# Performance work log

Measured on AMD Instinct MI355X. Metric: run time of the kernel, lower is better.

## Reference

```python
import jax, jax.numpy as jnp
import numpy as np

N, E, G = 50000, 800000, 64
NODE_DIM, HID, HEADS, EDGE_DIM = 128, 256, 4, 2
LAYER_IN = [NODE_DIM, HID, HID]
LAYER_HEADS = [HEADS, HEADS, 1]
BN_EPS = 1e-5


def setup_inputs() -> dict:
    key = jax.random.key(0)
    ks = iter(jax.random.split(key, 80))
    def nrm(shape, s=0.05):
        return jax.random.normal(next(ks), shape, jnp.float32) * s
    inp = {}
    inp['x'] = jax.random.normal(next(ks), (N, NODE_DIM), jnp.float32)
    inp['edge_index'] = jax.random.randint(next(ks), (2, E), 0, N, jnp.int32)
    inp['edge_attr'] = jax.random.normal(next(ks), (E, EDGE_DIM), jnp.float32)
    inp['batch'] = jnp.sort(jax.random.randint(next(ks), (N,), 0, G, jnp.int32))
    for i in range(3):
        H = LAYER_HEADS[i]; C = HID // H
        inp[f'W{i}'] = nrm((LAYER_IN[i], H * C))
        inp[f'asrc{i}'] = nrm((H, C))
        inp[f'adst{i}'] = nrm((H, C))
        inp[f'We{i}'] = nrm((EDGE_DIM, H * C))
        inp[f'aedge{i}'] = nrm((H, C))
        inp[f'bconv{i}'] = jnp.zeros((HID,), jnp.float32)
        inp[f'bn{i}_g'] = jnp.ones((HID,), jnp.float32)
        inp[f'bn{i}_b'] = jnp.zeros((HID,), jnp.float32)
        inp[f'bn{i}_m'] = nrm((HID,), 0.01)
        inp[f'bn{i}_v'] = jnp.ones((HID,), jnp.float32)
    inp['Wskip'] = nrm((NODE_DIM, HID))
    inp['bskip'] = jnp.zeros((HID,), jnp.float32)
    inp['Wp1'] = nrm((2 * HID, HID))
    inp['bp1'] = jnp.zeros((HID,), jnp.float32)
    inp['Wp2'] = nrm((HID, 1))
    inp['bp2'] = jnp.zeros((1,), jnp.float32)
    return inp


def gat_conv(x, src, dst, ea, W, a_s, a_d, We, a_e, b, H, concat):
    n = x.shape[0]
    C = W.shape[1] // H
    h = (x @ W).reshape(n, H, C)                      # [N,H,C]
    # attention logits per edge (src/dst node terms + edge term)
    al = ((h * a_s).sum(-1)[src]
          + (h * a_d).sum(-1)[dst]
          + ((ea @ We).reshape(-1, H, C) * a_e).sum(-1))  # [Et,H]
    al = jax.nn.leaky_relu(al, 0.2)
    # segment softmax over destination nodes
    amax = jax.ops.segment_max(al, dst, num_segments=n)
    ex = jnp.exp(al - amax[dst])
    den = jax.ops.segment_sum(ex, dst, num_segments=n)
    alpha = ex / (den[dst] + 1e-16)
    out = jax.ops.segment_sum(h[src] * alpha[..., None], dst, num_segments=n)  # [N,H,C]
    out = out.reshape(n, H * C) if concat else out.mean(axis=1)
    return out + b


def _forward(x, edge_index, edge_attr, batch, layer_params, Wskip, bskip, Wp1, bp1, Wp2, bp2):
    n = x.shape[0]
    # add self-loops (PyG GATConv default), edge_attr filled with mean
    loop = jnp.arange(n, dtype=edge_index.dtype)
    src = jnp.concatenate([edge_index[0], loop])
    dst = jnp.concatenate([edge_index[1], loop])
    ea = jnp.concatenate([edge_attr, jnp.broadcast_to(edge_attr.mean(0), (n, edge_attr.shape[1]))], axis=0)
    identity = x
    for i, (W, a_s, a_d, We, a_e, b, g, be, rm, rv) in enumerate(layer_params):
        layer_identity = (identity @ Wskip + bskip) if i == 0 else identity
        concat = i < 2
        H = LAYER_HEADS[i]
        h = gat_conv(x, src, dst, ea, W, a_s, a_d, We, a_e, b, H, concat)
        h = (h - rm) * jax.lax.rsqrt(rv + BN_EPS) * g + be   # BatchNorm1d (eval)
        h = jax.nn.elu(h)
        x = h + layer_identity
        identity = x
    # global mean + max pool per graph
    counts = jnp.maximum(jax.ops.segment_sum(jnp.ones((n,), x.dtype), batch, num_segments=G), 1.0)
    mean_pool = jax.ops.segment_sum(x, batch, num_segments=G) / counts[:, None]
    max_pool = jax.ops.segment_max(x, batch, num_segments=G)
    emb = jnp.concatenate([mean_pool, max_pool], axis=1)      # [G, 2*HID]
    hmid = jax.nn.relu(emb @ Wp1 + bp1)
    return hmid @ Wp2 + bp2                                   # [G, 1]


def reference(x, edge_index, edge_attr, batch,
              W0, asrc0, adst0, We0, aedge0, bconv0, bn0_g, bn0_b, bn0_m, bn0_v,
              W1, asrc1, adst1, We1, aedge1, bconv1, bn1_g, bn1_b, bn1_m, bn1_v,
              W2, asrc2, adst2, We2, aedge2, bconv2, bn2_g, bn2_b, bn2_m, bn2_v,
              Wskip, bskip, Wp1, bp1, Wp2, bp2):
    layer_params = [
        (W0, asrc0, adst0, We0, aedge0, bconv0, bn0_g, bn0_b, bn0_m, bn0_v),
        (W1, asrc1, adst1, We1, aedge1, bconv1, bn1_g, bn1_b, bn1_m, bn1_v),
        (W2, asrc2, adst2, We2, aedge2, bconv2, bn2_g, bn2_b, bn2_m, bn2_v),
    ]
    return _forward(x, edge_index, edge_attr, batch, layer_params, Wskip, bskip, Wp1, bp1, Wp2, bp2)
```

## Files before the change

kernel.cpp:

```cpp
#include <hip/hip_runtime.h>
#include <cfloat>

#define Nn 50000
#define Ee 800000
#define Etot (Ee + Nn)
#define Gg 64
#define HIDc 256
#define BN_EPS 1e-5f

typedef unsigned int   uint32;
typedef unsigned short ushort16;
typedef short  bf16x8 __attribute__((ext_vector_type(8)));
typedef float  f32x4  __attribute__((ext_vector_type(4)));

__device__ inline ushort16 f2bf(float f) {
    uint32 u = __float_as_uint(f);
    u = (u + 0x7fffu + ((u >> 16) & 1u)) >> 16;
    return (ushort16)u;
}
__device__ inline uint32 pack2(float a, float b) {
    return (uint32)f2bf(a) | ((uint32)f2bf(b) << 16);
}
__device__ inline uint32 fenc(float f) {
    uint32 b = __float_as_uint(f);
    return (b & 0x80000000u) ? ~b : (b | 0x80000000u);
}
__device__ inline float fdec(uint32 u) {
    uint32 b = (u & 0x80000000u) ? (u & 0x7fffffffu) : ~u;
    return __uint_as_float(b);
}

__device__ inline long ws_index(int c, int k, int KB) {
    int cb = c >> 4, m = c & 15, kb = k >> 5, q = (k >> 3) & 3, e = k & 7;
    return (((long)(cb * KB + kb) * 64 + q * 16 + m) << 3) + e;
}

#define CVT4 (Nn * 128 / 4)
#define CVT_BLKS ((CVT4 + 255) / 256)
#define EBKS ((Etot + 255) / 256)
__global__ __launch_bounds__(256) void prep_kernel(
        const float* __restrict__ ea, float* __restrict__ ea_s,
        const float* __restrict__ We0, const float* __restrict__ ae0,
        const float* __restrict__ We1, const float* __restrict__ ae1,
        const float* __restrict__ We2, const float* __restrict__ ae2,
        float* __restrict__ M,
        const float* __restrict__ W0, const float* __restrict__ Wskip,
        const float* __restrict__ W1, const float* __restrict__ W2,
        ushort16* __restrict__ WtC, ushort16* __restrict__ Wt1,
        ushort16* __restrict__ Wt2,
        const float* __restrict__ x, ushort16* __restrict__ xbf,
        const int* __restrict__ ei, int* __restrict__ counts) {
    int bid = blockIdx.x, t = threadIdx.x;
    if (bid < 256) {
        __shared__ float sh0[256], sh1[256];
        float s0 = 0.f, s1 = 0.f;
        for (int e = bid * 256 + t; e < Ee; e += 256 * 256) {
            s0 += ea[2 * e];
            s1 += ea[2 * e + 1];
        }
        sh0[t] = s0; sh1[t] = s1;
        __syncthreads();
        for (int off = 128; off > 0; off >>= 1) {
            if (t < off) { sh0[t] += sh0[t + off]; sh1[t] += sh1[t + off]; }
            __syncthreads();
        }
        if (t == 0) { atomicAdd(&ea_s[0], sh0[0]); atomicAdd(&ea_s[1], sh1[0]); }
    } else if (bid == 256) {
        if (t >= 18) return;
        int l = t < 8 ? 0 : (t < 16 ? 1 : 2);
        int r = t - l * 8;
        const float* We = (l == 0) ? We0 : (l == 1 ? We1 : We2);
        const float* ae = (l == 0) ? ae0 : (l == 1 ? ae1 : ae2);
        int Hl = (l < 2) ? 4 : 1;
        int Cl = 256 / Hl;
        int d = r / Hl, hh = r % Hl;
        float s = 0.f;
        for (int c = 0; c < Cl; ++c)
            s += We[d * 256 + hh * Cl + c] * ae[hh * Cl + c];
        M[l * 8 + r] = s;
    } else if (bid < 385) {
        int k = bid - 257;
        WtC[ws_index(t, k, 4)] = f2bf(W0[(long)k * 256 + t]);
    } else if (bid < 513) {
        int k = bid - 385;
        WtC[ws_index(256 + t, k, 4)] = f2bf(Wskip[(long)k * 256 + t]);
    } else if (bid < 769) {
        int k = bid - 513;
        Wt1[ws_index(t, k, 8)] = f2bf(W1[(long)k * 256 + t]);
    } else if (bid < 1025) {
        int k = bid - 769;
        Wt2[ws_index(t, k, 8)] = f2bf(W2[(long)k * 256 + t]);
    } else if (bid < 1025 + CVT_BLKS) {
        int i = (bid - 1025) * 256 + t;
        if (i < CVT4) {
            float4 v = *(const float4*)&x[i * 4];
            ushort4 o;
            o.x = f2bf(v.x); o.y = f2bf(v.y); o.z = f2bf(v.z); o.w = f2bf(v.w);
            *(ushort4*)&xbf[i * 4] = o;
        }
    } else {
        int e = (bid - 1025 - CVT_BLKS) * 256 + t;
        if (e < Etot) {
            int d = (e < Ee) ? ei[Ee + e] : (e - Ee);
            atomicAdd(&counts[d], 1);
        }
    }
}

__global__ void scan1_kernel(const int* __restrict__ in, int* __restrict__ inc,
                             int* __restrict__ bsums) {
    __shared__ int sh[256];
    int i = blockIdx.x * 256 + threadIdx.x;
    int v = (i < Nn) ? in[i] : 0;
    sh[threadIdx.x] = v;
    __syncthreads();
    for (int off = 1; off < 256; off <<= 1) {
        int t = ((int)threadIdx.x >= off) ? sh[threadIdx.x - off] : 0;
        __syncthreads();
        sh[threadIdx.x] += t;
        __syncthreads();
    }
    if (i < Nn) inc[i] = sh[threadIdx.x];
    if (threadIdx.x == 255) bsums[blockIdx.x] = sh[255];
}

__global__ void scan23_kernel(const int* __restrict__ inc, const int* __restrict__ bsums,
                              int* __restrict__ row_start, int* __restrict__ cursor, int nb) {
    __shared__ int sh[256];
    int b = blockIdx.x, t = threadIdx.x;
    sh[t] = (t < b && t < nb) ? bsums[t] : 0;
    __syncthreads();
    for (int off = 128; off > 0; off >>= 1) {
        if (t < off) sh[t] += sh[t + off];
        __syncthreads();
    }
    int base = sh[0];
    int i = b * 256 + t;
    if (i < Nn) {
        int v = inc[i] + base;
        row_start[i + 1] = v;
        cursor[i + 1] = v;
    }
    if (i == 0) { row_start[0] = 0; cursor[0] = 0; }
}

__global__ void scatter_kernel(const int* __restrict__ ei, const float* __restrict__ ea,
                               const float* __restrict__ ea_sum, int* __restrict__ cursor,
                               int* __restrict__ src_sorted, float* __restrict__ ea_sorted) {
    int e = blockIdx.x * blockDim.x + threadIdx.x;
    if (e >= Etot) return;
    int s, d; float e0, e1;
    if (e < Ee) {
        s = ei[e]; d = ei[Ee + e];
        e0 = ea[2 * e]; e1 = ea[2 * e + 1];
    } else {
        s = d = e - Ee;
        const float invE = 1.f / (float)Ee;
        e0 = ea_sum[0] * invE; e1 = ea_sum[1] * invE;
    }
    int pos = atomicAdd(&cursor[d], 1);
    src_sorted[pos] = s;
    ea_sorted[2 * pos]     = e0;
    ea_sorted[2 * pos + 1] = e1;
}

#define LDK 40
__global__ __launch_bounds__(256) void mfma_gemm_kernel(
        const ushort16* __restrict__ A,
        const ushort16* __restrict__ WS,
        uint32* __restrict__ outF,
        uint32* __restrict__ outS,
        const float* __restrict__ bskip,
        const float* __restrict__ a_s, const float* __restrict__ a_d,
        float* __restrict__ ssrc, float* __restrict__ sdst,
        int n, int K) {
    __shared__ ushort16 As[128 * LDK];
    const int t    = threadIdx.x;
    const int row0 = blockIdx.x * 128;
    const int c0   = blockIdx.y * 128;
    const bool isSkip = (outS != nullptr) && (c0 >= 256);
    const int cc0  = isSkip ? c0 - 256 : c0;
    const int wave = t >> 6, lane = t & 63;
    const int wr = wave >> 1, wc = wave & 1;
    const int l15 = lane & 15, quad = lane >> 4;
    const int KB = K >> 5;

    f32x4 acc[4][4];
#pragma unroll
    for (int j = 0; j < 4; ++j)
#pragma unroll
        for (int i = 0; i < 4; ++i) {
            acc[j][i][0] = 0.f; acc[j][i][1] = 0.f;
            acc[j][i][2] = 0.f; acc[j][i][3] = 0.f;
        }

    const int sm = t & 127;
    const int so = t >> 7;

    for (int k0 = 0; k0 < K; k0 += 32) {
        const int kb = k0 >> 5;
#pragma unroll
        for (int h = 0; h < 2; ++h) {
            int oct = so + 2 * h;
            int grow = row0 + sm;
            uint4 va = make_uint4(0, 0, 0, 0);
            if (grow < n) va = *(const uint4*)&A[(long)grow * K + k0 + 8 * oct];
            *(uint4*)&As[sm * LDK + 8 * oct] = va;
        }
        bf16x8 bfv[4];
#pragma unroll
        for (int j = 0; j < 4; ++j) {
            int cb = ((c0 + wc * 64) >> 4) + j;
            bfv[j] = *(const bf16x8*)&WS[(((long)cb * KB + kb) * 64 + lane) << 3];
        }
        __syncthreads();
        bf16x8 af[4];
#pragma unroll
        for (int i = 0; i < 4; ++i)
            af[i] = *(const bf16x8*)&As[(wr * 64 + i * 16 + l15) * LDK + quad * 8];
#pragma unroll
        for (int j = 0; j < 4; ++j)
#pragma unroll
            for (int i = 0; i < 4; ++i)
                acc[j][i] = __builtin_amdgcn_mfma_f32_16x16x32_bf16(
                    bfv[j], af[i], acc[j][i], 0, 0, 0);
        __syncthreads();
    }

    float4 bb[4];
#pragma unroll
    for (int j = 0; j < 4; ++j) {
        if (isSkip) bb[j] = *(const float4*)&bskip[cc0 + wc * 64 + j * 16 + quad * 4];
        else        bb[j] = make_float4(0.f, 0.f, 0.f, 0.f);
    }

    uint32* tgt = isSkip ? outS : outF;
#pragma unroll
    for (int i = 0; i < 4; ++i) {
        int row = row0 + wr * 64 + i * 16 + l15;
        if (row >= n) continue;
#pragma unroll
        for (int j = 0; j < 4; ++j) {
            int col = cc0 + wc * 64 + j * 16 + quad * 4;
            uint2 pk;
            pk.x = pack2(acc[j][i][0] + bb[j].x, acc[j][i][1] + bb[j].y);
            pk.y = pack2(acc[j][i][2] + bb[j].z, acc[j][i][3] + bb[j].w);
            *(uint2*)&tgt[(long)row * 128 + (col >> 1)] = pk;
        }
    }

    if (!isSkip && a_s != nullptr) {
        float4 asv[4], adv[4];
#pragma unroll
        for (int j = 0; j < 4; ++j) {
            int col = cc0 + wc * 64 + j * 16 + quad * 4;
            asv[j] = *(const float4*)&a_s[col];
            adv[j] = *(const float4*)&a_d[col];
        }
        const int part = (cc0 + wc * 64) >> 6;
#pragma unroll
        for (int i = 0; i < 4; ++i) {
            float ps = 0.f, pd = 0.f;
#pragma unroll
            for (int j = 0; j < 4; ++j) {
                ps += acc[j][i][0] * asv[j].x + acc[j][i][1] * asv[j].y
                    + acc[j][i][2] * asv[j].z + acc[j][i][3] * asv[j].w;
                pd += acc[j][i][0] * adv[j].x + acc[j][i][1] * adv[j].y
                    + acc[j][i][2] * adv[j].z + acc[j][i][3] * adv[j].w;
            }
            ps += __shfl_xor(ps, 16); ps += __shfl_xor(ps, 32);
            pd += __shfl_xor(pd, 16); pd += __shfl_xor(pd, 32);
            if (quad == 0) {
                int row = row0 + wr * 64 + i * 16 + l15;
                if (row < n) {
                    ssrc[row * 4 + part] = ps;
                    sdst[row * 4 + part] = pd;
                }
            }
        }
    }
}

template <int H>
__global__ __launch_bounds__(256) void edge_softmax_kernel(
        const int* __restrict__ src_sorted, const int* __restrict__ row_start,
        const float* __restrict__ ea_sorted, const float* __restrict__ ssrc,
        const float* __restrict__ sdst, const float* __restrict__ M,
        float* __restrict__ w) {
    int node = (blockIdx.x * blockDim.x + threadIdx.x) >> 4;
    int l16 = threadIdx.x & 15;
    if (node >= Nn) return;
    int beg = row_start[node], end = row_start[node + 1];
    int deg = end - beg;
    float sd[H], M0[H], M1[H], m[H], den[H];
    if (H == 4) {
#pragma unroll
        for (int h = 0; h < H; ++h) sd[h] = sdst[node * 4 + h];
    } else {
        float4 v = *(const float4*)&sdst[node * 4];
        sd[0] = v.x + v.y + v.z + v.w;
    }
#pragma unroll
    for (int h = 0; h < H; ++h) {
        M0[h] = M[h]; M1[h] = M[H + h];
        m[h] = -FLT_MAX; den[h] = 0.f;
    }
    auto ssval = [&](int s, int h) -> float {
        if (H == 4) return ssrc[s * 4 + h];
        float4 v = *(const float4*)&ssrc[s * 4];
        return v.x + v.y + v.z + v.w;
    };
    if (deg <= 64) {
        float lreg[4][H];
#pragma unroll
        for (int k = 0; k < 4; ++k) {
            int idx = beg + l16 + (k << 4);
            if (idx < end) {
                int s = src_sorted[idx];
                float e0 = ea_sorted[2 * idx], e1 = ea_sorted[2 * idx + 1];
#pragma unroll
                for (int h = 0; h < H; ++h) {
                    float l = ssval(s, h) + sd[h] + e0 * M0[h] + e1 * M1[h];
                    l = (l > 0.f) ? l : 0.2f * l;
                    lreg[k][h] = l;
                    if (l > m[h]) { den[h] = den[h] * __expf(m[h] - l) + 1.f; m[h] = l; }
                    else den[h] += __expf(l - m[h]);
                }
            }
        }
#pragma unroll
        for (int h = 0; h < H; ++h) {
#pragma unroll
            for (int off = 1; off < 16; off <<= 1) {
                float om = __shfl_xor(m[h], off);
                float od = __shfl_xor(den[h], off);
                float nm = fmaxf(m[h], om);
                den[h] = den[h] * __expf(m[h] - nm) + od * __expf(om - nm);
                m[h] = nm;
            }
            den[h] = 1.f / (den[h] + 1e-16f);
        }
#pragma unroll
        for (int k = 0; k < 4; ++k) {
            int idx = beg + l16 + (k << 4);
            if (idx < end) {
#pragma unroll
                for (int h = 0; h < H; ++h)
                    w[(long)idx * H + h] = __expf(lreg[k][h] - m[h]) * den[h];
            }
        }
    } else {
        for (int idx = beg + l16; idx < end; idx += 16) {
            int s = src_sorted[idx];
            float e0 = ea_sorted[2 * idx], e1 = ea_sorted[2 * idx + 1];
#pragma unroll
            for (int h = 0; h < H; ++h) {
                float l = ssval(s, h) + sd[h] + e0 * M0[h] + e1 * M1[h];
                l = (l > 0.f) ? l : 0.2f * l;
                w[(long)idx * H + h] = l;
                if (l > m[h]) { den[h] = den[h] * __expf(m[h] - l) + 1.f; m[h] = l; }
                else den[h] += __expf(l - m[h]);
            }
        }
#pragma unroll
        for (int h = 0; h < H; ++h) {
#pragma unroll
            for (int off = 1; off < 16; off <<= 1) {
                float om = __shfl_xor(m[h], off);
                float od = __shfl_xor(den[h], off);
                float nm = fmaxf(m[h], om);
                den[h] = den[h] * __expf(m[h] - nm) + od * __expf(om - nm);
                m[h] = nm;
            }
            den[h] = 1.f / (den[h] + 1e-16f);
        }
        for (int idx = beg + l16; idx < end; idx += 16) {
#pragma unroll
            for (int h = 0; h < H; ++h) {
                float l = w[(long)idx * H + h];
                w[(long)idx * H + h] = __expf(l - m[h]) * den[h];
            }
        }
    }
}

__global__ __launch_bounds__(128) void agg_kernel(
        const int* __restrict__ src_sorted, const int* __restrict__ row_start,
        const uint32* __restrict__ hbuf2, const float* __restrict__ w,
        const float* __restrict__ bconv,
        const float* __restrict__ bn_g, const float* __restrict__ bn_b,
        const float* __restrict__ bn_m, const float* __restrict__ bn_v,
        const uint32* __restrict__ identity2, uint32* __restrict__ out2, int H) {
    int node = blockIdx.x;
    int c2 = threadIdx.x;
    int C2 = 128 / H;
    int hh = c2 / C2;
    int beg = row_start[node], end = row_start[node + 1];
    float a0 = 0.f, a1 = 0.f;
    for (int idx = beg; idx < end; idx += 4) {
        int   s[4];
        float ww[4];
#pragma unroll
        for (int k = 0; k < 4; ++k) {
            int j = idx + k;
            bool ok = j < end;
            int jj = ok ? j : beg;
            s[k]  = src_sorted[jj];
            ww[k] = ok ? w[(long)jj * H + hh] : 0.f;
        }
#pragma unroll
        for (int k = 0; k < 4; ++k) {
            uint32 u = hbuf2[(long)s[k] * 128 + c2];
            float lo = __uint_as_float(u << 16);
            float hi = __uint_as_float(u & 0xffff0000u);
            a0 += ww[k] * lo;
            a1 += ww[k] * hi;
        }
    }
    int c = 2 * c2;
    float v0 = a0 + bconv[c];
    float v1 = a1 + bconv[c + 1];
    v0 = (v0 - bn_m[c])     * rsqrtf(bn_v[c]     + BN_EPS) * bn_g[c]     + bn_b[c];
    v1 = (v1 - bn_m[c + 1]) * rsqrtf(bn_v[c + 1] + BN_EPS) * bn_g[c + 1] + bn_b[c + 1];
    v0 = (v0 > 0.f) ? v0 : (expf(v0) - 1.f);
    v1 = (v1 > 0.f) ? v1 : (expf(v1) - 1.f);
    uint32 idu = identity2[(long)node * 128 + c2];
    v0 += __uint_as_float(idu << 16);
    v1 += __uint_as_float(idu & 0xffff0000u);
    out2[(long)node * 128 + c2] = pack2(v0, v1);
}

#define POOL_ROWS 32
__global__ __launch_bounds__(128) void pool_kernel(
        const uint32* __restrict__ x2, const int* __restrict__ batch,
        float* __restrict__ psum, uint32* __restrict__ pmax, float* __restrict__ pcnt) {
    int c2 = threadIdx.x;
    int n0 = blockIdx.x * POOL_ROWS;
    if (n0 >= Nn) return;
    int n1 = min(n0 + POOL_ROWS, Nn);
    int cur = batch[n0];
    float s0 = 0.f, s1 = 0.f, m0 = -FLT_MAX, m1 = -FLT_MAX;
    int cnt = 0;
    int c = 2 * c2;
    for (int i = n0; i < n1; ++i) {
        int g = batch[i];
        if (g != cur) {
            atomicAdd(&psum[cur * 256 + c], s0);
            atomicAdd(&psum[cur * 256 + c + 1], s1);
            atomicMax(&pmax[cur * 256 + c], fenc(m0));
            atomicMax(&pmax[cur * 256 + c + 1], fenc(m1));
            if (c2 == 0) atomicAdd(&pcnt[cur], (float)cnt);
            cur = g; s0 = s1 = 0.f; m0 = m1 = -FLT_MAX; cnt = 0;
        }
        uint32 u = x2[(long)i * 128 + c2];
        float lo = __uint_as_float(u << 16);
        float hi = __uint_as_float(u & 0xffff0000u);
        s0 += lo; s1 += hi;
        m0 = fmaxf(m0, lo); m1 = fmaxf(m1, hi);
        ++cnt;
    }
    atomicAdd(&psum[cur * 256 + c], s0);
    atomicAdd(&psum[cur * 256 + c + 1], s1);
    atomicMax(&pmax[cur * 256 + c], fenc(m0));
    atomicMax(&pmax[cur * 256 + c + 1], fenc(m1));
    if (c2 == 0) atomicAdd(&pcnt[cur], (float)cnt);
}

__global__ __launch_bounds__(256) void mlp_kernel(
        const float* __restrict__ psum, const uint32* __restrict__ pmax,
        const float* __restrict__ pcnt, const float* __restrict__ Wp1,
        const float* __restrict__ bp1, const float* __restrict__ Wp2,
        const float* __restrict__ bp2, float* __restrict__ out) {
    int g = blockIdx.x;
    int j = threadIdx.x;
    float inv = 1.f / fmaxf(pcnt[g], 1.f);
    float acc = bp1[j];
    for (int k = 0; k < 256; ++k)
        acc += (psum[g * 256 + k] * inv) * Wp1[k * 256 + j];
    for (int k = 0; k < 256; ++k)
        acc += fdec(pmax[g * 256 + k]) * Wp1[(256 + k) * 256 + j];
    float v = fmaxf(acc, 0.f) * Wp2[j];
    __shared__ float red[256];
    red[j] = v;
    __syncthreads();
    for (int off = 128; off > 0; off >>= 1) {
        if (j < off) red[j] += red[j + off];
        __syncthreads();
    }
    if (j == 0) out[g] = red[0] + bp2[0];
}

extern "C" void kernel_launch(void* const* d_in, const int* in_sizes, int n_in,
                              void* d_out, int out_size, void* d_ws, size_t ws_size,
                              hipStream_t stream) {
    const float* x   = (const float*)d_in[0];
    const int*   ei  = (const int*)d_in[1];
    const float* ea  = (const float*)d_in[2];
    const int*   bat = (const int*)d_in[3];
    auto LP = [&](int l, int j) { return (const float*)d_in[4 + l * 10 + j]; };
    const float* Wskip = (const float*)d_in[34];
    const float* bskip = (const float*)d_in[35];
    const float* Wp1   = (const float*)d_in[36];
    const float* bp1   = (const float*)d_in[37];
    const float* Wp2   = (const float*)d_in[38];
    const float* bp2   = (const float*)d_in[39];
    float* out = (float*)d_out;

    char* p = (char*)d_ws;
    auto alloc = [&](size_t bytes) { void* r = (void*)p; p += (bytes + 255) & ~(size_t)255; return r; };
    uint32*   hbuf2  = (uint32*)alloc((size_t)Nn * 256 * 2);
    uint32*   skipbf = (uint32*)alloc((size_t)Nn * 128 * 4);
    uint32*   resA   = (uint32*)alloc((size_t)Nn * 128 * 4);
    uint32*   resB   = (uint32*)alloc((size_t)Nn * 128 * 4);
    ushort16* xbf    = (ushort16*)alloc((size_t)Nn * 128 * 2);
    float*    wbuf   = (float*)alloc((size_t)Etot * 4 * 4);
    float*    ea_sorted = (float*)alloc((size_t)Etot * 2 * 4);
    float*    ssrc   = (float*)alloc((size_t)Nn * 4 * 4);
    float*    sdst   = (float*)alloc((size_t)Nn * 4 * 4);
    int*      counts = (int*)alloc((size_t)Nn * 4);
    int*      incb   = (int*)alloc((size_t)Nn * 4);
    int*      row_start = (int*)alloc((size_t)(Nn + 1) * 4);
    int*      cursor    = (int*)alloc((size_t)(Nn + 1) * 4);
    int*      src_sorted = (int*)alloc((size_t)Etot * 4);
    int*      bsums  = (int*)alloc(256 * 4);
    float*    ea_s   = (float*)alloc(2 * 4);
    float*    Mbuf   = (float*)alloc(32 * 4);
    ushort16* WtC    = (ushort16*)alloc((size_t)512 * 128 * 2);
    ushort16* Wt1    = (ushort16*)alloc((size_t)256 * 256 * 2);
    ushort16* Wt2    = (ushort16*)alloc((size_t)256 * 256 * 2);
    float*    psum   = (float*)alloc((size_t)Gg * 256 * 4);
    uint32*   pmax   = (uint32*)alloc((size_t)Gg * 256 * 4);
    float*    pcnt   = (float*)alloc((size_t)Gg * 4);

    const int nb = (Nn + 255) / 256;
    const int sgrid = (Nn * 16 + 255) / 256;

    hipMemsetAsync(counts, 0, (size_t)Nn * 4, stream);
    hipMemsetAsync(ea_s, 0, 8, stream);
    hipMemsetAsync(psum, 0, (size_t)Gg * 256 * 4 * 2 + (size_t)Gg * 4, stream);

    prep_kernel<<<1025 + CVT_BLKS + EBKS, 256, 0, stream>>>(
        ea, ea_s, LP(0,3), LP(0,4), LP(1,3), LP(1,4), LP(2,3), LP(2,4), Mbuf,
        LP(0,0), Wskip, LP(1,0), LP(2,0), WtC, Wt1, Wt2, x, xbf, ei, counts);

    scan1_kernel<<<nb, 256, 0, stream>>>(counts, incb, bsums);
    scan23_kernel<<<nb, 256, 0, stream>>>(incb, bsums, row_start, cursor, nb);
    scatter_kernel<<<EBKS, 256, 0, stream>>>(ei, ea, ea_s, cursor, src_sorted, ea_sorted);

    {
        dim3 g0((Nn + 127) / 128, 4);
        mfma_gemm_kernel<<<g0, 256, 0, stream>>>(
            xbf, WtC, hbuf2, skipbf, bskip,
            LP(0,1), LP(0,2), ssrc, sdst, Nn, 128);
    }

    const uint32* lid[3] = { skipbf, resA, resB };
    uint32*       lou[3] = { resA, resB, resA };
    const int     Hh[3]  = { 4, 4, 1 };
    const ushort16* lain[3] = { nullptr, (ushort16*)resA, (ushort16*)resB };
    const ushort16* lwt[3]  = { nullptr, Wt1, Wt2 };
    for (int l = 0; l < 3; ++l) {
        const int H = Hh[l];
        if (l > 0) {
            dim3 gl((Nn + 127) / 128, 2);
            mfma_gemm_kernel<<<gl, 256, 0, stream>>>(
                lain[l], lwt[l], hbuf2, nullptr, nullptr,
                LP(l,1), LP(l,2), ssrc, sdst, Nn, 256);
        }
        if (H == 4)
            edge_softmax_kernel<4><<<sgrid, 256, 0, stream>>>(
                src_sorted, row_start, ea_sorted, ssrc, sdst, Mbuf + l * 8, wbuf);
        else
            edge_softmax_kernel<1><<<sgrid, 256, 0, stream>>>(
                src_sorted, row_start, ea_sorted, ssrc, sdst, Mbuf + l * 8, wbuf);
        agg_kernel<<<Nn, 128, 0, stream>>>(src_sorted, row_start, hbuf2, wbuf,
            LP(l,5), LP(l,6), LP(l,7), LP(l,8), LP(l,9), lid[l], lou[l], H);
    }

    pool_kernel<<<(Nn + POOL_ROWS - 1) / POOL_ROWS, 128, 0, stream>>>(resA, bat, psum, pmax, pcnt);
    mlp_kernel<<<Gg, 256, 0, stream>>>(psum, pmax, pcnt, Wp1, bp1, Wp2, bp2, out);
}
```

Before: 669.0 us.

## Aggregate one node per wavefront with 8-byte loads and deeper unroll

The aggregation kernel now maps one 64-lane wavefront per destination node, with four nodes per 256-thread block, instead of one 128-thread block per node. Each lane loads two packed bf16 pairs (uint2) and accumulates four channels, and the edge loop is unrolled by 8 to keep more gathers in flight. The aim is less per-block launch and scheduling overhead, wider memory transactions and more memory-level parallelism in the gather-bound loop. Register pressure rises, and wavefronts in the same block finish unevenly when node degrees differ.

```diff
diff --git a/kernel.cpp b/kernel.cpp
--- a/kernel.cpp
+++ b/kernel.cpp
@@ -384,50 +384,68 @@
     }
 }
 
-__global__ __launch_bounds__(128) void agg_kernel(
+#define AGG_UNROLL 8
+__global__ __launch_bounds__(256) void agg_kernel(
         const int* __restrict__ src_sorted, const int* __restrict__ row_start,
         const uint32* __restrict__ hbuf2, const float* __restrict__ w,
         const float* __restrict__ bconv,
         const float* __restrict__ bn_g, const float* __restrict__ bn_b,
         const float* __restrict__ bn_m, const float* __restrict__ bn_v,
         const uint32* __restrict__ identity2, uint32* __restrict__ out2, int H) {
-    int node = blockIdx.x;
-    int c2 = threadIdx.x;
-    int C2 = 128 / H;
-    int hh = c2 / C2;
+    int wv = threadIdx.x >> 6;
+    int l  = threadIdx.x & 63;
+    int node = blockIdx.x * 4 + wv;
+    if (node >= Nn) return;
+    int lanesPerHead = 64 / H;
+    int hh = l / lanesPerHead;
     int beg = row_start[node], end = row_start[node + 1];
-    float a0 = 0.f, a1 = 0.f;
-    for (int idx = beg; idx < end; idx += 4) {
-        int   s[4];
-        float ww[4];
-#pragma unroll
-        for (int k = 0; k < 4; ++k) {
+    float a0 = 0.f, a1 = 0.f, a2 = 0.f, a3 = 0.f;
+    for (int idx = beg; idx < end; idx += AGG_UNROLL) {
+        int   s[AGG_UNROLL];
+        float ww[AGG_UNROLL];
+#pragma unroll
+        for (int k = 0; k < AGG_UNROLL; ++k) {
             int j = idx + k;
             bool ok = j < end;
-            int jj = ok ? j : beg;
+            int jj = ok ? j : (end - 1);
             s[k]  = src_sorted[jj];
             ww[k] = ok ? w[(long)jj * H + hh] : 0.f;
         }
 #pragma unroll
-        for (int k = 0; k < 4; ++k) {
-            uint32 u = hbuf2[(long)s[k] * 128 + c2];
-            float lo = __uint_as_float(u << 16);
-            float hi = __uint_as_float(u & 0xffff0000u);
-            a0 += ww[k] * lo;
-            a1 += ww[k] * hi;
-        }
-    }
-    int c = 2 * c2;
-    float v0 = a0 + bconv[c];
-    float v1 = a1 + bconv[c + 1];
-    v0 = (v0 - bn_m[c])     * rsqrtf(bn_v[c]     + BN_EPS) * bn_g[c]     + bn_b[c];
-    v1 = (v1 - bn_m[c + 1]) * rsqrtf(bn_v[c + 1] + BN_EPS) * bn_g[c + 1] + bn_b[c + 1];
+        for (int k = 0; k < AGG_UNROLL; ++k) {
+            uint2 u = *(const uint2*)&hbuf2[(long)s[k] * 128 + 2 * l];
+            float f0 = __uint_as_float(u.x << 16);
+            float f1 = __uint_as_float(u.x & 0xffff0000u);
+            float f2 = __uint_as_float(u.y << 16);
+            float f3 = __uint_as_float(u.y & 0xffff0000u);
+            a0 += ww[k] * f0; a1 += ww[k] * f1;
+            a2 += ww[k] * f2; a3 += ww[k] * f3;
+        }
+    }
+    int c = 4 * l;
+    float4 bcv = *(const float4*)&bconv[c];
+    float4 bgv = *(const float4*)&bn_g[c];
+    float4 bbv = *(const float4*)&bn_b[c];
+    float4 bmv = *(const float4*)&bn_m[c];
+    float4 bvv = *(const float4*)&bn_v[c];
+    float v0 = a0 + bcv.x, v1 = a1 + bcv.y, v2 = a2 + bcv.z, v3 = a3 + bcv.w;
+    v0 = (v0 - bmv.x) * rsqrtf(bvv.x + BN_EPS) * bgv.x + bbv.x;
+    v1 = (v1 - bmv.y) * rsqrtf(bvv.y + BN_EPS) * bgv.y + bbv.y;
+    v2 = (v2 - bmv.z) * rsqrtf(bvv.z + BN_EPS) * bgv.z + bbv.z;
+    v3 = (v3 - bmv.w) * rsqrtf(bvv.w + BN_EPS) * bgv.w + bbv.w;
     v0 = (v0 > 0.f) ? v0 : (expf(v0) - 1.f);
     v1 = (v1 > 0.f) ? v1 : (expf(v1) - 1.f);
-    uint32 idu = identity2[(long)node * 128 + c2];
-    v0 += __uint_as_float(idu << 16);
-    v1 += __uint_as_float(idu & 0xffff0000u);
-    out2[(long)node * 128 + c2] = pack2(v0, v1);
+    v2 = (v2 > 0.f) ? v2 : (expf(v2) - 1.f);
+    v3 = (v3 > 0.f) ? v3 : (expf(v3) - 1.f);
+    uint2 idu = *(const uint2*)&identity2[(long)node * 128 + 2 * l];
+    v0 += __uint_as_float(idu.x << 16);
+    v1 += __uint_as_float(idu.x & 0xffff0000u);
+    v2 += __uint_as_float(idu.y << 16);
+    v3 += __uint_as_float(idu.y & 0xffff0000u);
+    uint2 o;
+    o.x = pack2(v0, v1);
+    o.y = pack2(v2, v3);
+    *(uint2*)&out2[(long)node * 128 + 2 * l] = o;
 }
 
 #define POOL_ROWS 32
@@ -573,7 +591,7 @@
         else
             edge_softmax_kernel<1><<<sgrid, 256, 0, stream>>>(
                 src_sorted, row_start, ea_sorted, ssrc, sdst, Mbuf + l * 8, wbuf);
-        agg_kernel<<<Nn, 128, 0, stream>>>(src_sorted, row_start, hbuf2, wbuf,
+        agg_kernel<<<(Nn + 3) / 4, 256, 0, stream>>>(src_sorted, row_start, hbuf2, wbuf,
             LP(l,5), LP(l,6), LP(l,7), LP(l,8), LP(l,9), lid[l], lou[l], H);
     }
 
```

Measured after the change: 666.3 us. No clear change (-0.4%).
